# Performance work log

Hardware: AMD Instinct MI355X
Metric: run time of the kernel (lower is better)

The kernel has to match this reference:

```python
import jax, jax.numpy as jnp
import numpy as np

B, S, T, E, H = 2, 2048, 2048, 1024, 16
D = E // H  # head_dim = 64


def setup_inputs() -> dict:
    key = jax.random.key(0)
    ks = jax.random.split(key, 11)
    scale = 1.0 / np.sqrt(E)
    return {
        "query": jax.random.normal(ks[0], (B, S, E), jnp.float32),
        "value": jax.random.normal(ks[1], (B, T, E), jnp.float32),
        "key": jax.random.normal(ks[2], (B, T, E), jnp.float32),
        "Wq": jax.random.normal(ks[3], (E, E), jnp.float32) * scale,
        "bq": jnp.zeros((E,), jnp.float32),
        "Wk": jax.random.normal(ks[4], (E, E), jnp.float32) * scale,
        "bk": jnp.zeros((E,), jnp.float32),
        "Wv": jax.random.normal(ks[5], (E, E), jnp.float32) * scale,
        "bv": jnp.zeros((E,), jnp.float32),
        "Wo": jax.random.normal(ks[6], (E, E), jnp.float32) * scale,
        "bo": jnp.zeros((E,), jnp.float32),
    }


def reference(query, value, key, Wq, bq, Wk, bk, Wv, bv, Wo, bo):
    b, s, e = query.shape
    t = value.shape[1]
    # linear projections (torch Linear: x @ W.T + b)
    q = query @ Wq.T + bq
    k = key @ Wk.T + bk
    v = value @ Wv.T + bv
    # split heads: [B, H, S, D]
    q = q.reshape(b, s, H, D).transpose(0, 2, 1, 3)
    k = k.reshape(b, t, H, D).transpose(0, 2, 1, 3)
    v = v.reshape(b, t, H, D).transpose(0, 2, 1, 3)
    # scaled dot-product attention; full [B,H,S,T] scores as in the original
    A = jnp.einsum("bhsd,bhtd->bhst", q, k) / jnp.sqrt(jnp.float32(D))
    A = jax.nn.softmax(A, axis=-1)
    # dropout p=0.0 -> identity
    out = jnp.einsum("bhst,bhtd->bhsd", A, v)
    out = out.transpose(0, 2, 1, 3).reshape(b, s, e)
    return out @ Wo.T + bo
```

## Files before the change

kernel.cpp:

```cpp
#include <hip/hip_runtime.h>
#include <math.h>

typedef __attribute__((ext_vector_type(8))) short short8;
typedef __attribute__((ext_vector_type(4))) float f32x4;
typedef __attribute__((ext_vector_type(16))) float f32x16;
typedef unsigned short u16;

__device__ __forceinline__ u16 f2bf(float x) {
    unsigned int u = __float_as_uint(x);
    u += 0x7FFFu + ((u >> 16) & 1u);
    return (u16)(u >> 16);
}

__device__ __forceinline__ unsigned cvt_pk_bf16(float lo, float hi) {
    unsigned r;
    asm("v_cvt_pk_bf16_f32 %0, %1, %2" : "=v"(r) : "v"(lo), "v"(hi));
    return r;
}

__device__ __forceinline__ float max3f(float a, float b, float c) {
    float r;
    asm("v_max3_f32 %0, %1, %2, %3" : "=v"(r) : "v"(a), "v"(b), "v"(c));
    return r;
}

__device__ __forceinline__ void load_lds16(const void* g, void* l) {
    __builtin_amdgcn_global_load_lds(
        (const __attribute__((address_space(1))) unsigned int*)g,
        (__attribute__((address_space(3))) unsigned int*)l,
        16, 0, 0);
}

struct CvtArgs {
    const float* src[7];
    u16* dst[7];
    int n8[7];
};

__global__ __launch_bounds__(256) void cvt_bf16(CvtArgs c) {
    const int z = blockIdx.z;
    const int i = blockIdx.x * 256 + threadIdx.x;
    if (i >= c.n8[z]) return;
    const float4* s = (const float4*)c.src[z];
    const float4 a = s[2 * i];
    const float4 b = s[2 * i + 1];
    union { short8 v; unsigned u[4]; } o;
    o.u[0] = cvt_pk_bf16(a.x, a.y);
    o.u[1] = cvt_pk_bf16(a.z, a.w);
    o.u[2] = cvt_pk_bf16(b.x, b.y);
    o.u[3] = cvt_pk_bf16(b.z, b.w);
    ((short8*)c.dst[z])[i] = o.v;
}

struct GemmArgs {
    const u16* A[3];
    const u16* W[3];
    const float* bias[3];
    void* C[3];
    float scale[3];
    int trans[3];
};

template <bool BF16OUT>
__global__ __launch_bounds__(256) void gemm_nt_mfma(GemmArgs ga, int M, int N, int K)
{
    __shared__ u16 As[2][128 * 32];
    __shared__ u16 Bs[2][128 * 32];
    const int z = blockIdx.z;
    const u16* __restrict__ A = ga.A[z];
    const u16* __restrict__ W = ga.W[z];
    const float* __restrict__ bias = ga.bias[z];
    const float scale = ga.scale[z];
    const int trans = ga.trans[z];

    const int tid = threadIdx.x;
    const int w = tid >> 6, l = tid & 63;
    const int l4 = l >> 4, lm = l & 15;
    const int wr = w >> 1, wc = w & 1;

    const int idx = blockIdx.x;
    const int xcd = idx & 7;
    const int sl  = idx >> 3;
    const int bmi = xcd * 4 + (sl & 3);
    const int bni = sl >> 2;
    const int bm = (trans ? bni : bmi) * 128;
    const int bn = (trans ? bmi : bni) * 128;

    const int srow = l >> 2;
    const int sseg = l & 3;

    f32x4 acc[4][4];
#pragma unroll
    for (int m = 0; m < 4; ++m)
#pragma unroll
        for (int n = 0; n < 4; ++n) acc[m][n] = (f32x4){0.f, 0.f, 0.f, 0.f};

    auto stage = [&](int k0, int bi) {
#pragma unroll
        for (int i = 0; i < 2; ++i) {
            const int blk = w * 2 + i;
            const int row = blk * 16 + srow;
            load_lds16(A + (size_t)(bm + row) * K + k0 + sseg * 8,
                       (char*)&As[bi][0] + blk * 1024);
            load_lds16(W + (size_t)(bn + row) * K + k0 + sseg * 8,
                       (char*)&Bs[bi][0] + blk * 1024);
        }
    };

    const int nIt = K / 32;
    stage(0, 0);

    for (int it = 0; it < nIt; ++it) {
        const int buf = it & 1;
        if (it < nIt - 1) {
            stage((it + 1) * 32, buf ^ 1);
            asm volatile("s_waitcnt vmcnt(4)" ::: "memory");
        } else {
            asm volatile("s_waitcnt vmcnt(0)" ::: "memory");
        }
        __builtin_amdgcn_s_barrier();

        short8 af[4], bf[4];
#pragma unroll
        for (int m = 0; m < 4; ++m)
            af[m] = *(const short8*)&As[buf][(wr * 64 + m * 16 + lm) * 32 + l4 * 8];
#pragma unroll
        for (int n = 0; n < 4; ++n)
            bf[n] = *(const short8*)&Bs[buf][(wc * 64 + n * 16 + lm) * 32 + l4 * 8];
#pragma unroll
        for (int m = 0; m < 4; ++m)
#pragma unroll
            for (int n = 0; n < 4; ++n)
                acc[m][n] = __builtin_amdgcn_mfma_f32_16x16x32_bf16(af[m], bf[n], acc[m][n], 0, 0, 0);

        __builtin_amdgcn_s_barrier();
    }

    if (!trans) {
        float bv[4];
#pragma unroll
        for (int n = 0; n < 4; ++n) bv[n] = bias[bn + wc * 64 + n * 16 + lm];
#pragma unroll
        for (int m = 0; m < 4; ++m) {
#pragma unroll
            for (int n = 0; n < 4; ++n) {
                const int col = bn + wc * 64 + n * 16 + lm;
#pragma unroll
                for (int r = 0; r < 4; ++r) {
                    const int row = bm + wr * 64 + m * 16 + l4 * 4 + r;
                    const float v = (acc[m][n][r] + bv[n]) * scale;
                    if (BF16OUT)
                        ((u16*)ga.C[z])[(size_t)row * N + col] = f2bf(v);
                    else
                        ((float*)ga.C[z])[(size_t)row * N + col] = v;
                }
            }
        }
    } else {
#pragma unroll
        for (int m = 0; m < 4; ++m) {
            const float4 bv4 = *(const float4*)(bias + bm + wr * 64 + m * 16 + l4 * 4);
            const float bvr[4] = {bv4.x, bv4.y, bv4.z, bv4.w};
#pragma unroll
            for (int n = 0; n < 4; ++n) {
                const int col = bn + wc * 64 + n * 16 + lm;
                const size_t cbase = (size_t)(col >> 11) * 2097152 + (size_t)(col & 2047);
#pragma unroll
                for (int r = 0; r < 4; ++r) {
                    const int row = bm + wr * 64 + m * 16 + l4 * 4 + r;
                    const float v = (acc[m][n][r] + bvr[r]) * scale;
                    ((u16*)ga.C[z])[cbase + (size_t)row * 2048] = f2bf(v);
                }
            }
        }
    }
}

__global__ __launch_bounds__(256, 2) void flash_attn_mfma9(
    const u16* __restrict__ Qb, const u16* __restrict__ Kb,
    const u16* __restrict__ Vt, u16* __restrict__ Ob)
{
    __shared__ u16 Ks[2][128 * 64];
    __shared__ u16 Vs[2][64 * 128];

    const int tid = threadIdx.x;
    const int w  = tid >> 6;
    const int l  = tid & 63;
    const int hi = l >> 5;
    const int lq = l & 31;

    const int id = blockIdx.x;
    const int xcd = id & 7;
    const int s = id >> 3;
    const int qt = s & 15;
    const int g0 = (s >> 4) * 8 + xcd;
    const int h = g0 & 15;
    const int b = g0 >> 4;
    const int qb0 = qt << 7;

    const size_t bbase = (size_t)b * 2048 * 1024 + (size_t)h * 64;
    const size_t vbase = (size_t)b * 2097152 + (size_t)(h * 64) * 2048;

    short8 qf[4];
    {
        const u16* qrow = Qb + bbase + (size_t)(qb0 + w * 32 + lq) * 1024;
#pragma unroll
        for (int t = 0; t < 4; ++t)
            qf[t] = *(const short8*)(qrow + t * 16 + hi * 8);
    }

    auto stageK = [&](int t0, int bufi) {
#pragma unroll
        for (int ii = 0; ii < 4; ++ii) {
            const int i = w * 4 + ii;
            const int key = i * 8 + (l >> 3);
            const int chunk = (l & 7) ^ ((l >> 3) & 7);
            load_lds16(Kb + bbase + (size_t)(t0 + key) * 1024 + chunk * 8,
                       (char*)&Ks[bufi][0] + i * 1024);
        }
    };
    auto stageV = [&](int t0, int bufi) {
#pragma unroll
        for (int ii = 0; ii < 4; ++ii) {
            const int i = w * 4 + ii;
            const int d = i * 4 + (l >> 4);
            const int chunk = (l & 15) ^ (d & 7);
            load_lds16(Vt + vbase + (size_t)d * 2048 + t0 + chunk * 8,
                       (char*)&Vs[bufi][0] + i * 1024);
        }
    };

    f32x16 oacc[2] = {{}, {}};
    float m_run = -1e30f;
    float l_run = 0.f;

    stageK(0, 0);
    stageV(0, 0);

    for (int t = 0; t < 16; ++t) {
        const int buf = t & 1;
        if (t < 15) {
            stageK((t + 1) * 128, buf ^ 1);
            stageV((t + 1) * 128, buf ^ 1);
            asm volatile("s_waitcnt vmcnt(8)" ::: "memory");
        } else {
            asm volatile("s_waitcnt vmcnt(0)" ::: "memory");
        }
        __builtin_amdgcn_s_barrier();

        f32x16 sacc[4] = {{}, {}, {}, {}};
        __builtin_amdgcn_s_setprio(1);
#pragma unroll
        for (int kb = 0; kb < 4; ++kb) {
#pragma unroll
            for (int tt = 0; tt < 4; ++tt) {
                const short8 kf = *(const short8*)
                    &Ks[buf][(32 * kb + lq) * 64 + (((2 * tt + hi) ^ (l & 7)) << 3)];
                sacc[kb] = __builtin_amdgcn_mfma_f32_32x32x16_bf16(kf, qf[tt], sacc[kb], 0, 0, 0);
            }
        }
        __builtin_amdgcn_s_setprio(0);

        float amax[4];
#pragma unroll
        for (int kb = 0; kb < 4; ++kb) {
            const f32x16 sv = sacc[kb];
            float t0 = max3f(sv[0], sv[1], sv[2]);
            float t1 = max3f(sv[3], sv[4], sv[5]);
            float t2 = max3f(sv[6], sv[7], sv[8]);
            float t3 = max3f(sv[9], sv[10], sv[11]);
            float t4 = max3f(sv[12], sv[13], sv[14]);
            float u0 = max3f(t0, t1, t2);
            float u1 = max3f(t3, t4, sv[15]);
            amax[kb] = fmaxf(u0, u1);
        }
        float mt = fmaxf(max3f(amax[0], amax[1], amax[2]), amax[3]);
        mt = fmaxf(mt, __shfl_xor(mt, 32));

        const bool resc = !__all(mt <= m_run + 8.0f);
        if (resc) {
            const float mn = fmaxf(m_run, mt);
            const float alpha = __builtin_amdgcn_exp2f(m_run - mn);
            m_run = mn;
            l_run *= alpha;
#pragma unroll
            for (int r = 0; r < 16; ++r) {
                const float a = __shfl(alpha, (r & 3) + 8 * (r >> 2) + 4 * hi);
                oacc[0][r] *= a;
                oacc[1][r] *= a;
            }
        }

        float lsum = 0.f;
        const float mr = m_run;
        unsigned wlo[4][4], whi[4][4];
#pragma unroll
        for (int kb = 0; kb < 4; ++kb) {
#pragma unroll
            for (int qd = 0; qd < 4; ++qd) {
                const float p0 = __builtin_amdgcn_exp2f(sacc[kb][4 * qd + 0] - mr);
                const float p1 = __builtin_amdgcn_exp2f(sacc[kb][4 * qd + 1] - mr);
                const float p2 = __builtin_amdgcn_exp2f(sacc[kb][4 * qd + 2] - mr);
                const float p3 = __builtin_amdgcn_exp2f(sacc[kb][4 * qd + 3] - mr);
                lsum += (p0 + p1) + (p2 + p3);
                wlo[kb][qd] = cvt_pk_bf16(p0, p1);
                whi[kb][qd] = cvt_pk_bf16(p2, p3);
            }
        }
        lsum += __shfl_xor(lsum, 32);
        l_run += lsum;

#pragma unroll
        for (int kb = 0; kb < 4; ++kb) {
#pragma unroll
            for (int u = 0; u < 2; ++u) {
                unsigned X  = wlo[kb][2 * u], Y  = wlo[kb][2 * u + 1];
                unsigned X2 = whi[kb][2 * u], Y2 = whi[kb][2 * u + 1];
                asm("v_permlane32_swap_b32 %0, %1" : "+v"(X),  "+v"(Y));
                asm("v_permlane32_swap_b32 %0, %1" : "+v"(X2), "+v"(Y2));
                union { unsigned u4[4]; short8 v8; } pa;
                pa.u4[0] = X; pa.u4[1] = X2; pa.u4[2] = Y; pa.u4[3] = Y2;
                const int sstep = 2 * kb + u;
                __builtin_amdgcn_s_setprio(1);
#pragma unroll
                for (int g = 0; g < 2; ++g) {
                    const int d = 32 * g + lq;
                    const short8 vf = *(const short8*)
                        &Vs[buf][d * 128 + (((2 * sstep + hi) ^ (d & 7)) << 3)];
                    oacc[g] = __builtin_amdgcn_mfma_f32_32x32x16_bf16(pa.v8, vf, oacc[g], 0, 0, 0);
                }
                __builtin_amdgcn_s_setprio(0);
            }
        }

        __builtin_amdgcn_s_barrier();
    }

#pragma unroll
    for (int r = 0; r < 16; ++r) {
        const int row = (r & 3) + 8 * (r >> 2) + 4 * hi;
        const float linv = 1.f / __shfl(l_run, row);
        const size_t orow = bbase + (size_t)(qb0 + w * 32 + row) * 1024;
        Ob[orow + lq]      = f2bf(oacc[0][r] * linv);
        Ob[orow + 32 + lq] = f2bf(oacc[1][r] * linv);
    }
}

extern "C" void kernel_launch(void* const* d_in, const int* in_sizes, int n_in,
                              void* d_out, int out_size, void* d_ws, size_t ws_size,
                              hipStream_t stream)
{
    const float* query = (const float*)d_in[0];
    const float* value = (const float*)d_in[1];
    const float* key   = (const float*)d_in[2];
    const float* Wq = (const float*)d_in[3];
    const float* bq = (const float*)d_in[4];
    const float* Wk = (const float*)d_in[5];
    const float* bk = (const float*)d_in[6];
    const float* Wv = (const float*)d_in[7];
    const float* bv = (const float*)d_in[8];
    const float* Wo = (const float*)d_in[9];
    const float* bo = (const float*)d_in[10];
    float* out = (float*)d_out;

    const int M = 2 * 2048;
    const int E = 1024;
    const size_t act = (size_t)M * E;
    const size_t wel = (size_t)E * E;

    u16* qc  = (u16*)d_ws;
    u16* kc  = qc + act;
    u16* vc  = kc + act;
    u16* wqb = vc + act;
    u16* wkb = wqb + wel;
    u16* wvb = wkb + wel;
    u16* wob = wvb + wel;
    u16* Qb  = wob + wel;
    u16* Kb  = Qb + act;
    u16* Vtb = Kb + act;
    u16* Ab  = Vtb + act;

    CvtArgs ca;
    ca.src[0] = query; ca.dst[0] = qc;  ca.n8[0] = (int)(act / 8);
    ca.src[1] = key;   ca.dst[1] = kc;  ca.n8[1] = (int)(act / 8);
    ca.src[2] = value; ca.dst[2] = vc;  ca.n8[2] = (int)(act / 8);
    ca.src[3] = Wq;    ca.dst[3] = wqb; ca.n8[3] = (int)(wel / 8);
    ca.src[4] = Wk;    ca.dst[4] = wkb; ca.n8[4] = (int)(wel / 8);
    ca.src[5] = Wv;    ca.dst[5] = wvb; ca.n8[5] = (int)(wel / 8);
    ca.src[6] = Wo;    ca.dst[6] = wob; ca.n8[6] = (int)(wel / 8);
    dim3 cgrid((unsigned)((act / 8 + 255) / 256), 1, 7);
    hipLaunchKernelGGL(cvt_bf16, cgrid, dim3(256), 0, stream, ca);

    const float SCALE_Q = 0.125f * 1.4426950408889634f;

    GemmArgs gq;
    gq.A[0] = qc;  gq.W[0] = wqb; gq.bias[0] = bq; gq.C[0] = Qb;  gq.scale[0] = SCALE_Q; gq.trans[0] = 0;
    gq.A[1] = kc;  gq.W[1] = wkb; gq.bias[1] = bk; gq.C[1] = Kb;  gq.scale[1] = 1.0f;    gq.trans[1] = 0;
    gq.A[2] = wvb; gq.W[2] = vc;  gq.bias[2] = bv; gq.C[2] = Vtb; gq.scale[2] = 1.0f;    gq.trans[2] = 1;
    hipLaunchKernelGGL((gemm_nt_mfma<true>), dim3(256, 1, 3), dim3(256), 0, stream, gq, M, E, E);

    hipLaunchKernelGGL(flash_attn_mfma9, dim3(512), dim3(256), 0, stream, Qb, Kb, Vtb, Ab);

    GemmArgs go;
    go.A[0] = Ab; go.W[0] = wob; go.bias[0] = bo; go.C[0] = out; go.scale[0] = 1.0f; go.trans[0] = 0;
    go.A[1] = Ab; go.W[1] = wob; go.bias[1] = bo; go.C[1] = out; go.scale[1] = 1.0f; go.trans[1] = 0;
    go.A[2] = Ab; go.W[2] = wob; go.bias[2] = bo; go.C[2] = out; go.scale[2] = 1.0f; go.trans[2] = 0;
    hipLaunchKernelGGL((gemm_nt_mfma<false>), dim3(256, 1, 1), dim3(256), 0, stream, go, M, E, E);
}
```

Before: 137.6 us.

## Fuse fp32-to-bf16 conversion into QKV projection GEMM loads

Removes the separate conversion pass over the query/key/value activations and the Wq/Wk/Wv weights. A new GEMM kernel loads fp32 tiles into registers, converts them to bf16 and writes them to LDS through a register-staged double buffer. Only Wo is still converted in a standalone kernel. This saves a full write and re-read of the bf16 copies, but the GEMM now reads twice as many bytes per tile and gives up the direct global-to-LDS async loads.

```diff
diff --git a/kernel.cpp b/kernel.cpp
--- a/kernel.cpp
+++ b/kernel.cpp
@@ -31,17 +31,11 @@
         16, 0, 0);
 }
 
-struct CvtArgs {
-    const float* src[7];
-    u16* dst[7];
-    int n8[7];
-};
-
-__global__ __launch_bounds__(256) void cvt_bf16(CvtArgs c) {
-    const int z = blockIdx.z;
+__global__ __launch_bounds__(256) void cvt_one(const float* __restrict__ src,
+                                               u16* __restrict__ dst, int n8) {
     const int i = blockIdx.x * 256 + threadIdx.x;
-    if (i >= c.n8[z]) return;
-    const float4* s = (const float4*)c.src[z];
+    if (i >= n8) return;
+    const float4* s = (const float4*)src;
     const float4 a = s[2 * i];
     const float4 b = s[2 * i + 1];
     union { short8 v; unsigned u[4]; } o;
@@ -49,7 +43,151 @@
     o.u[1] = cvt_pk_bf16(a.z, a.w);
     o.u[2] = cvt_pk_bf16(b.x, b.y);
     o.u[3] = cvt_pk_bf16(b.z, b.w);
-    ((short8*)c.dst[z])[i] = o.v;
+    ((short8*)dst)[i] = o.v;
+}
+
+struct GemmArgsF {
+    const float* A[3];
+    const float* W[3];
+    const float* bias[3];
+    void* C[3];
+    float scale[3];
+    int trans[3];
+};
+
+__global__ __launch_bounds__(256) void gemm_nt_f32(GemmArgsF ga, int M, int N, int K)
+{
+    __shared__ u16 As[2][128 * 32];
+    __shared__ u16 Bs[2][128 * 32];
+    const int z = blockIdx.z;
+    const float* __restrict__ A = ga.A[z];
+    const float* __restrict__ W = ga.W[z];
+    const float* __restrict__ bias = ga.bias[z];
+    const float scale = ga.scale[z];
+    const int trans = ga.trans[z];
+
+    const int tid = threadIdx.x;
+    const int w = tid >> 6, l = tid & 63;
+    const int l4 = l >> 4, lm = l & 15;
+    const int wr = w >> 1, wc = w & 1;
+
+    const int idx = blockIdx.x;
+    const int xcd = idx & 7;
+    const int sl  = idx >> 3;
+    const int bmi = xcd * 4 + (sl & 3);
+    const int bni = sl >> 2;
+    const int bm = (trans ? bni : bmi) * 128;
+    const int bn = (trans ? bmi : bni) * 128;
+
+    const int r0 = tid >> 2;
+    const int c8 = (tid & 3) * 8;
+
+    f32x4 acc[4][4];
+#pragma unroll
+    for (int m = 0; m < 4; ++m)
+#pragma unroll
+        for (int n = 0; n < 4; ++n) acc[m][n] = (f32x4){0.f, 0.f, 0.f, 0.f};
+
+    float4 aR[2][2], wR[2][2];
+    auto load_regs = [&](int k0) {
+#pragma unroll
+        for (int j = 0; j < 2; ++j) {
+            const int row = r0 + j * 64;
+            const float* p = A + (size_t)(bm + row) * K + k0 + c8;
+            aR[j][0] = *(const float4*)p;
+            aR[j][1] = *(const float4*)(p + 4);
+            const float* q = W + (size_t)(bn + row) * K + k0 + c8;
+            wR[j][0] = *(const float4*)q;
+            wR[j][1] = *(const float4*)(q + 4);
+        }
+    };
+    auto write_tile = [&](int bi) {
+#pragma unroll
+        for (int j = 0; j < 2; ++j) {
+            const int row = r0 + j * 64;
+            union { short8 v; unsigned u[4]; } o;
+            o.u[0] = cvt_pk_bf16(aR[j][0].x, aR[j][0].y);
+            o.u[1] = cvt_pk_bf16(aR[j][0].z, aR[j][0].w);
+            o.u[2] = cvt_pk_bf16(aR[j][1].x, aR[j][1].y);
+            o.u[3] = cvt_pk_bf16(aR[j][1].z, aR[j][1].w);
+            *(short8*)&As[bi][row * 32 + c8] = o.v;
+            union { short8 v; unsigned u[4]; } p;
+            p.u[0] = cvt_pk_bf16(wR[j][0].x, wR[j][0].y);
+            p.u[1] = cvt_pk_bf16(wR[j][0].z, wR[j][0].w);
+            p.u[2] = cvt_pk_bf16(wR[j][1].x, wR[j][1].y);
+            p.u[3] = cvt_pk_bf16(wR[j][1].z, wR[j][1].w);
+            *(short8*)&Bs[bi][row * 32 + c8] = p.v;
+        }
+    };
+
+    const int nIt = K / 32;
+    load_regs(0);
+    asm volatile("s_waitcnt vmcnt(0)" ::: "memory");
+    write_tile(0);
+    load_regs(32);
+    __builtin_amdgcn_s_barrier();
+
+    for (int it = 0; it < nIt; ++it) {
+        const int buf = it & 1;
+
+        short8 af[4], bf[4];
+#pragma unroll
+        for (int m = 0; m < 4; ++m)
+            af[m] = *(const short8*)&As[buf][(wr * 64 + m * 16 + lm) * 32 + l4 * 8];
+#pragma unroll
+        for (int n = 0; n < 4; ++n)
+            bf[n] = *(const short8*)&Bs[buf][(wc * 64 + n * 16 + lm) * 32 + l4 * 8];
+        __builtin_amdgcn_s_setprio(1);
+#pragma unroll
+        for (int m = 0; m < 4; ++m)
+#pragma unroll
+            for (int n = 0; n < 4; ++n)
+                acc[m][n] = __builtin_amdgcn_mfma_f32_16x16x32_bf16(af[m], bf[n], acc[m][n], 0, 0, 0);
+        __builtin_amdgcn_s_setprio(0);
+
+        if (it < nIt - 1) {
+            asm volatile("s_waitcnt vmcnt(0)" ::: "memory");
+            write_tile(buf ^ 1);
+            if (it < nIt - 2) load_regs((it + 2) * 32);
+        }
+        __builtin_amdgcn_s_barrier();
+    }
+
+    if (!trans) {
+        float bv[4];
+#pragma unroll
+        for (int n = 0; n < 4; ++n) bv[n] = bias[bn + wc * 64 + n * 16 + lm];
+#pragma unroll
+        for (int m = 0; m < 4; ++m) {
+#pragma unroll
+            for (int n = 0; n < 4; ++n) {
+                const int col = bn + wc * 64 + n * 16 + lm;
+#pragma unroll
+                for (int r = 0; r < 4; ++r) {
+                    const int row = bm + wr * 64 + m * 16 + l4 * 4 + r;
+                    const float v = (acc[m][n][r] + bv[n]) * scale;
+                    ((u16*)ga.C[z])[(size_t)row * N + col] = f2bf(v);
+                }
+            }
+        }
+    } else {
+#pragma unroll
+        for (int m = 0; m < 4; ++m) {
+            const float4 bv4 = *(const float4*)(bias + bm + wr * 64 + m * 16 + l4 * 4);
+            const float bvr[4] = {bv4.x, bv4.y, bv4.z, bv4.w};
+#pragma unroll
+            for (int n = 0; n < 4; ++n) {
+                const int col = bn + wc * 64 + n * 16 + lm;
+                const size_t cbase = (size_t)(col >> 11) * 2097152 + (size_t)(col & 2047);
+#pragma unroll
+                for (int r = 0; r < 4; ++r) {
+                    const int row = bm + wr * 64 + m * 16 + l4 * 4 + r;
+                    const float v = (acc[m][n][r] + bvr[r]) * scale;
+                    ((u16*)ga.C[z])[cbase + (size_t)row * 2048] = f2bf(v);
+                }
+            }
+        }
+    }
 }
 
 struct GemmArgs {
@@ -368,36 +506,22 @@
     const size_t act = (size_t)M * E;
     const size_t wel = (size_t)E * E;
 
-    u16* qc  = (u16*)d_ws;
-    u16* kc  = qc + act;
-    u16* vc  = kc + act;
-    u16* wqb = vc + act;
-    u16* wkb = wqb + wel;
-    u16* wvb = wkb + wel;
-    u16* wob = wvb + wel;
+    u16* wob = (u16*)d_ws;
     u16* Qb  = wob + wel;
     u16* Kb  = Qb + act;
     u16* Vtb = Kb + act;
     u16* Ab  = Vtb + act;
 
-    CvtArgs ca;
-    ca.src[0] = query; ca.dst[0] = qc;  ca.n8[0] = (int)(act / 8);
-    ca.src[1] = key;   ca.dst[1] = kc;  ca.n8[1] = (int)(act / 8);
-    ca.src[2] = value; ca.dst[2] = vc;  ca.n8[2] = (int)(act / 8);
-    ca.src[3] = Wq;    ca.dst[3] = wqb; ca.n8[3] = (int)(wel / 8);
-    ca.src[4] = Wk;    ca.dst[4] = wkb; ca.n8[4] = (int)(wel / 8);
-    ca.src[5] = Wv;    ca.dst[5] = wvb; ca.n8[5] = (int)(wel / 8);
-    ca.src[6] = Wo;    ca.dst[6] = wob; ca.n8[6] = (int)(wel / 8);
-    dim3 cgrid((unsigned)((act / 8 + 255) / 256), 1, 7);
-    hipLaunchKernelGGL(cvt_bf16, cgrid, dim3(256), 0, stream, ca);
+    hipLaunchKernelGGL(cvt_one, dim3((unsigned)(wel / 8 / 256)), dim3(256), 0, stream,
+                       Wo, wob, (int)(wel / 8));
 
     const float SCALE_Q = 0.125f * 1.4426950408889634f;
 
-    GemmArgs gq;
-    gq.A[0] = qc;  gq.W[0] = wqb; gq.bias[0] = bq; gq.C[0] = Qb;  gq.scale[0] = SCALE_Q; gq.trans[0] = 0;
-    gq.A[1] = kc;  gq.W[1] = wkb; gq.bias[1] = bk; gq.C[1] = Kb;  gq.scale[1] = 1.0f;    gq.trans[1] = 0;
-    gq.A[2] = wvb; gq.W[2] = vc;  gq.bias[2] = bv; gq.C[2] = Vtb; gq.scale[2] = 1.0f;    gq.trans[2] = 1;
-    hipLaunchKernelGGL((gemm_nt_mfma<true>), dim3(256, 1, 3), dim3(256), 0, stream, gq, M, E, E);
+    GemmArgsF gq;
+    gq.A[0] = query; gq.W[0] = Wq;    gq.bias[0] = bq; gq.C[0] = Qb;  gq.scale[0] = SCALE_Q; gq.trans[0] = 0;
+    gq.A[1] = key;   gq.W[1] = Wk;    gq.bias[1] = bk; gq.C[1] = Kb;  gq.scale[1] = 1.0f;    gq.trans[1] = 0;
+    gq.A[2] = Wv;    gq.W[2] = value; gq.bias[2] = bv; gq.C[2] = Vtb; gq.scale[2] = 1.0f;    gq.trans[2] = 1;
+    hipLaunchKernelGGL(gemm_nt_f32, dim3(256, 1, 3), dim3(256), 0, stream, gq, M, E, E);
 
     hipLaunchKernelGGL(flash_attn_mfma9, dim3(512), dim3(256), 0, stream, Qb, Kb, Vtb, Ab);
 
```

After: 154.5 us. +12.3%, slower.

## Fuse fp32-to-bf16 activation conversion into QKV projection GEMM loads

Applied to the files above, without the earlier changes.

The separate conversion pass over the query, key and value activations is removed. The QKV GEMM now stages fp32 activation tiles straight into LDS with an XOR swizzle and converts them to bf16 in registers before the MFMA, which saves a full write and reread of the activations. The V-transpose output is now written as vectorized ushort4 stores, and the MFMA section is wrapped in s_setprio. In exchange the kernel uses twice the LDS for the A tile and adds per-iteration conversion ALU work.

```diff
diff --git a/kernel.cpp b/kernel.cpp
--- a/kernel.cpp
+++ b/kernel.cpp
@@ -32,9 +32,9 @@
 }
 
 struct CvtArgs {
-    const float* src[7];
-    u16* dst[7];
-    int n8[7];
+    const float* src[4];
+    u16* dst[4];
+    int n8[4];
 };
 
 __global__ __launch_bounds__(256) void cvt_bf16(CvtArgs c) {
@@ -52,22 +52,21 @@
     ((short8*)c.dst[z])[i] = o.v;
 }
 
-struct GemmArgs {
-    const u16* A[3];
+struct GemmArgsF {
+    const float* A[3];
     const u16* W[3];
     const float* bias[3];
-    void* C[3];
+    u16* C[3];
     float scale[3];
     int trans[3];
 };
 
-template <bool BF16OUT>
-__global__ __launch_bounds__(256) void gemm_nt_mfma(GemmArgs ga, int M, int N, int K)
+__global__ __launch_bounds__(256) void gemm_nt_af32(GemmArgsF ga, int M, int N, int K)
 {
-    __shared__ u16 As[2][128 * 32];
-    __shared__ u16 Bs[2][128 * 32];
+    __shared__ float As[2][128 * 32];
+    __shared__ u16   Bs[2][128 * 32];
     const int z = blockIdx.z;
-    const u16* __restrict__ A = ga.A[z];
+    const float* __restrict__ A = ga.A[z];
     const u16* __restrict__ W = ga.W[z];
     const float* __restrict__ bias = ga.bias[z];
     const float scale = ga.scale[z];
@@ -83,8 +82,141 @@
     const int sl  = idx >> 3;
     const int bmi = xcd * 4 + (sl & 3);
     const int bni = sl >> 2;
-    const int bm = (trans ? bni : bmi) * 128;
-    const int bn = (trans ? bmi : bni) * 128;
+    const int bm = bmi * 128;
+    const int bn = bni * 128;
+
+    const int srow = l >> 2;
+    const int sseg = l & 3;
+    const int arowi = l >> 3;
+    const int achunk = (l & 7) ^ (arowi & 7);
+
+    f32x4 acc[4][4];
+#pragma unroll
+    for (int m = 0; m < 4; ++m)
+#pragma unroll
+        for (int n = 0; n < 4; ++n) acc[m][n] = (f32x4){0.f, 0.f, 0.f, 0.f};
+
+    auto stage = [&](int k0, int bi) {
+#pragma unroll
+        for (int ii = 0; ii < 4; ++ii) {
+            const int blk = w * 4 + ii;
+            const int row = blk * 8 + arowi;
+            load_lds16(A + (size_t)(bm + row) * K + k0 + achunk * 4,
+                       (char*)&As[bi][0] + blk * 1024);
+        }
+#pragma unroll
+        for (int i = 0; i < 2; ++i) {
+            const int blk = w * 2 + i;
+            const int row = blk * 16 + srow;
+            load_lds16(W + (size_t)(bn + row) * K + k0 + sseg * 8,
+                       (char*)&Bs[bi][0] + blk * 1024);
+        }
+    };
+
+    const int nIt = K / 32;
+    stage(0, 0);
+
+    for (int it = 0; it < nIt; ++it) {
+        const int buf = it & 1;
+        if (it < nIt - 1) {
+            stage((it + 1) * 32, buf ^ 1);
+            asm volatile("s_waitcnt vmcnt(6)" ::: "memory");
+        } else {
+            asm volatile("s_waitcnt vmcnt(0)" ::: "memory");
+        }
+        __builtin_amdgcn_s_barrier();
+
+        short8 af[4];
+#pragma unroll
+        for (int m = 0; m < 4; ++m) {
+            const int arow = wr * 64 + m * 16 + lm;
+            const f32x4 a0 = *(const f32x4*)&As[buf][arow * 32 + (((2 * l4)     ^ (arow & 7)) << 2)];
+            const f32x4 a1 = *(const f32x4*)&As[buf][arow * 32 + (((2 * l4 + 1) ^ (arow & 7)) << 2)];
+            union { short8 v; unsigned u[4]; } o;
+            o.u[0] = cvt_pk_bf16(a0.x, a0.y);
+            o.u[1] = cvt_pk_bf16(a0.z, a0.w);
+            o.u[2] = cvt_pk_bf16(a1.x, a1.y);
+            o.u[3] = cvt_pk_bf16(a1.z, a1.w);
+            af[m] = o.v;
+        }
+        short8 bf[4];
+#pragma unroll
+        for (int n = 0; n < 4; ++n)
+            bf[n] = *(const short8*)&Bs[buf][(wc * 64 + n * 16 + lm) * 32 + l4 * 8];
+
+        __builtin_amdgcn_s_setprio(1);
+#pragma unroll
+        for (int m = 0; m < 4; ++m)
+#pragma unroll
+            for (int n = 0; n < 4; ++n)
+                acc[m][n] = __builtin_amdgcn_mfma_f32_16x16x32_bf16(af[m], bf[n], acc[m][n], 0, 0, 0);
+        __builtin_amdgcn_s_setprio(0);
+
+        __builtin_amdgcn_s_barrier();
+    }
+
+    float bv[4];
+#pragma unroll
+    for (int n = 0; n < 4; ++n) bv[n] = bias[bn + wc * 64 + n * 16 + lm];
+
+    if (!trans) {
+#pragma unroll
+        for (int m = 0; m < 4; ++m) {
+#pragma unroll
+            for (int n = 0; n < 4; ++n) {
+                const int col = bn + wc * 64 + n * 16 + lm;
+#pragma unroll
+                for (int r = 0; r < 4; ++r) {
+                    const int row = bm + wr * 64 + m * 16 + l4 * 4 + r;
+                    ga.C[z][(size_t)row * N + col] = f2bf((acc[m][n][r] + bv[n]) * scale);
+                }
+            }
+        }
+    } else {
+#pragma unroll
+        for (int m = 0; m < 4; ++m) {
+            const int tok = bm + wr * 64 + m * 16 + l4 * 4;
+#pragma unroll
+            for (int n = 0; n < 4; ++n) {
+                const int dim = bn + wc * 64 + n * 16 + lm;
+                const size_t base = (size_t)(tok >> 11) * 2097152
+                                  + (size_t)dim * 2048 + (tok & 2047);
+                ushort4 o;
+                o.x = f2bf((acc[m][n][0] + bv[n]) * scale);
+                o.y = f2bf((acc[m][n][1] + bv[n]) * scale);
+                o.z = f2bf((acc[m][n][2] + bv[n]) * scale);
+                o.w = f2bf((acc[m][n][3] + bv[n]) * scale);
+                *(ushort4*)(ga.C[z] + base) = o;
+            }
+        }
+    }
+}
+
+struct GemmArgs {
+    const u16* A;
+    const u16* W;
+    const float* bias;
+    float* C;
+};
+
+__global__ __launch_bounds__(256) void gemm_nt_mfma(GemmArgs ga, int M, int N, int K)
+{
+    __shared__ u16 As[2][128 * 32];
+    __shared__ u16 Bs[2][128 * 32];
+    const u16* __restrict__ A = ga.A;
+    const u16* __restrict__ W = ga.W;
+    const float* __restrict__ bias = ga.bias;
+
+    const int tid = threadIdx.x;
+    const int w = tid >> 6, l = tid & 63;
+    const int l4 = l >> 4, lm = l & 15;
+    const int wr = w >> 1, wc = w & 1;
+
+    const int idx = blockIdx.x;
+    const int xcd = idx & 7;
+    const int sl  = idx >> 3;
+    const int bm = (xcd * 4 + (sl & 3)) * 128;
+    const int bn = (sl >> 2) * 128;
 
     const int srow = l >> 2;
     const int sseg = l & 3;
@@ -136,41 +268,18 @@
         __builtin_amdgcn_s_barrier();
     }
 
-    if (!trans) {
-        float bv[4];
-#pragma unroll
-        for (int n = 0; n < 4; ++n) bv[n] = bias[bn + wc * 64 + n * 16 + lm];
-#pragma unroll
-        for (int m = 0; m < 4; ++m) {
-#pragma unroll
-            for (int n = 0; n < 4; ++n) {
-                const int col = bn + wc * 64 + n * 16 + lm;
-#pragma unroll
-                for (int r = 0; r < 4; ++r) {
-                    const int row = bm + wr * 64 + m * 16 + l4 * 4 + r;
-                    const float v = (acc[m][n][r] + bv[n]) * scale;
-                    if (BF16OUT)
-                        ((u16*)ga.C[z])[(size_t)row * N + col] = f2bf(v);
-                    else
-                        ((float*)ga.C[z])[(size_t)row * N + col] = v;
-                }
-            }
-        }
-    } else {
-#pragma unroll
-        for (int m = 0; m < 4; ++m) {
-            const float4 bv4 = *(const float4*)(bias + bm + wr * 64 + m * 16 + l4 * 4);
-            const float bvr[4] = {bv4.x, bv4.y, bv4.z, bv4.w};
-#pragma unroll
-            for (int n = 0; n < 4; ++n) {
-                const int col = bn + wc * 64 + n * 16 + lm;
-                const size_t cbase = (size_t)(col >> 11) * 2097152 + (size_t)(col & 2047);
-#pragma unroll
-                for (int r = 0; r < 4; ++r) {
-                    const int row = bm + wr * 64 + m * 16 + l4 * 4 + r;
-                    const float v = (acc[m][n][r] + bvr[r]) * scale;
-                    ((u16*)ga.C[z])[cbase + (size_t)row * 2048] = f2bf(v);
-                }
+    float bv[4];
+#pragma unroll
+    for (int n = 0; n < 4; ++n) bv[n] = bias[bn + wc * 64 + n * 16 + lm];
+#pragma unroll
+    for (int m = 0; m < 4; ++m) {
+#pragma unroll
+        for (int n = 0; n < 4; ++n) {
+            const int col = bn + wc * 64 + n * 16 + lm;
+#pragma unroll
+            for (int r = 0; r < 4; ++r) {
+                const int row = bm + wr * 64 + m * 16 + l4 * 4 + r;
+                ga.C[(size_t)row * N + col] = acc[m][n][r] + bv[n];
             }
         }
     }
@@ -368,10 +477,7 @@
     const size_t act = (size_t)M * E;
     const size_t wel = (size_t)E * E;
 
-    u16* qc  = (u16*)d_ws;
-    u16* kc  = qc + act;
-    u16* vc  = kc + act;
-    u16* wqb = vc + act;
+    u16* wqb = (u16*)d_ws;
     u16* wkb = wqb + wel;
     u16* wvb = wkb + wel;
     u16* wob = wvb + wel;
@@ -381,29 +487,24 @@
     u16* Ab  = Vtb + act;
 
     CvtArgs ca;
-    ca.src[0] = query; ca.dst[0] = qc;  ca.n8[0] = (int)(act / 8);
-    ca.src[1] = key;   ca.dst[1] = kc;  ca.n8[1] = (int)(act / 8);
-    ca.src[2] = value; ca.dst[2] = vc;  ca.n8[2] = (int)(act / 8);
-    ca.src[3] = Wq;    ca.dst[3] = wqb; ca.n8[3] = (int)(wel / 8);
-    ca.src[4] = Wk;    ca.dst[4] = wkb; ca.n8[4] = (int)(wel / 8);
-    ca.src[5] = Wv;    ca.dst[5] = wvb; ca.n8[5] = (int)(wel / 8);
-    ca.src[6] = Wo;    ca.dst[6] = wob; ca.n8[6] = (int)(wel / 8);
-    dim3 cgrid((unsigned)((act / 8 + 255) / 256), 1, 7);
+    ca.src[0] = Wq; ca.dst[0] = wqb; ca.n8[0] = (int)(wel / 8);
+    ca.src[1] = Wk; ca.dst[1] = wkb; ca.n8[1] = (int)(wel / 8);
+    ca.src[2] = Wv; ca.dst[2] = wvb; ca.n8[2] = (int)(wel / 8);
+    ca.src[3] = Wo; ca.dst[3] = wob; ca.n8[3] = (int)(wel / 8);
+    dim3 cgrid((unsigned)((wel / 8 + 255) / 256), 1, 4);
     hipLaunchKernelGGL(cvt_bf16, cgrid, dim3(256), 0, stream, ca);
 
     const float SCALE_Q = 0.125f * 1.4426950408889634f;
 
-    GemmArgs gq;
-    gq.A[0] = qc;  gq.W[0] = wqb; gq.bias[0] = bq; gq.C[0] = Qb;  gq.scale[0] = SCALE_Q; gq.trans[0] = 0;
-    gq.A[1] = kc;  gq.W[1] = wkb; gq.bias[1] = bk; gq.C[1] = Kb;  gq.scale[1] = 1.0f;    gq.trans[1] = 0;
-    gq.A[2] = wvb; gq.W[2] = vc;  gq.bias[2] = bv; gq.C[2] = Vtb; gq.scale[2] = 1.0f;    gq.trans[2] = 1;
-    hipLaunchKernelGGL((gemm_nt_mfma<true>), dim3(256, 1, 3), dim3(256), 0, stream, gq, M, E, E);
+    GemmArgsF gq;
+    gq.A[0] = query; gq.W[0] = wqb; gq.bias[0] = bq; gq.C[0] = Qb;  gq.scale[0] = SCALE_Q; gq.trans[0] = 0;
+    gq.A[1] = key;   gq.W[1] = wkb; gq.bias[1] = bk; gq.C[1] = Kb;  gq.scale[1] = 1.0f;    gq.trans[1] = 0;
+    gq.A[2] = value; gq.W[2] = wvb; gq.bias[2] = bv; gq.C[2] = Vtb; gq.scale[2] = 1.0f;    gq.trans[2] = 1;
+    hipLaunchKernelGGL(gemm_nt_af32, dim3(256, 1, 3), dim3(256), 0, stream, gq, M, E, E);
 
     hipLaunchKernelGGL(flash_attn_mfma9, dim3(512), dim3(256), 0, stream, Qb, Kb, Vtb, Ab);
 
     GemmArgs go;
-    go.A[0] = Ab; go.W[0] = wob; go.bias[0] = bo; go.C[0] = out; go.scale[0] = 1.0f; go.trans[0] = 0;
-    go.A[1] = Ab; go.W[1] = wob; go.bias[1] = bo; go.C[1] = out; go.scale[1] = 1.0f; go.trans[1] = 0;
-    go.A[2] = Ab; go.W[2] = wob; go.bias[2] = bo; go.C[2] = out; go.scale[2] = 1.0f; go.trans[2] = 0;
-    hipLaunchKernelGGL((gemm_nt_mfma<false>), dim3(256, 1, 1), dim3(256), 0, stream, go, M, E, E);
-}
+    go.A = Ab; go.W = wob; go.bias = bo; go.C = out;
+    hipLaunchKernelGGL(gemm_nt_mfma, dim3(256), dim3(256), 0, stream, go, M, E, E);
+}
```

New measurement: 123.4 us, median of 2. 1.11x faster.
